# Kernel optimization log

Measured on AMD Instinct MI355X. Metric: run time of the kernel, lower is better.

The kernel has to match this reference:

```python
import jax, jax.numpy as jnp
import numpy as np
import math

N, V, NH = 4096, 256, 64  # samples, variables (channels), hidden units


def _permutation_skeleton(v):
    # perm[c] is a (V, V-1) selection matrix keeping all variables j != c,
    # columns ordered by j (faithful to CustomizedRelaModule.permutation_matrix
    # with skeleton = 1 - I, so max_dim = V - 1 and no zero-padding remains).
    perm = np.zeros((v, v, v - 1), dtype=np.float32)
    for c in range(v):
        idx = np.delete(np.arange(v), c)
        perm[c, idx, np.arange(v - 1)] = 1.0
    return jnp.asarray(perm)


def setup_inputs() -> dict:
    key = jax.random.key(0)
    k = jax.random.split(key, 7)
    data = jax.random.normal(k[0], (N, V), dtype=jnp.float32)
    adj = jax.random.normal(k[1], (V, V), dtype=jnp.float32)        # self.adj_matrix ~ N(0,1)
    neurons = jax.random.normal(k[2], (NH, V), dtype=jnp.float32)   # self.neurons ~ N(0,1)
    s1 = 1.0 / math.sqrt(V - 1)  # input_layer: uniform(-1/sqrt(in), 1/sqrt(in)), in = max_dim = V-1
    w_in = jax.random.uniform(k[3], (V, V - 1, NH), minval=-s1, maxval=s1, dtype=jnp.float32)
    b_in = jax.random.uniform(k[4], (V, NH), minval=-s1, maxval=s1, dtype=jnp.float32)
    s2 = 1.0 / math.sqrt(NH)
    w_out = jax.random.uniform(k[5], (V, NH, 1), minval=-s2, maxval=s2, dtype=jnp.float32)
    b_out = jax.random.uniform(k[6], (V, 1), minval=-s2, maxval=s2, dtype=jnp.float32)
    perm = _permutation_skeleton(V)
    return {"data": data, "adj": adj, "neurons": neurons,
            "w_in": w_in, "b_in": b_in, "w_out": w_out, "b_out": b_out,
            "perm": perm}


def reference(data, adj, neurons, w_in, b_in, w_out, b_out, perm):
    # categorical_matrix is identity, so the adjacency passed is adj itself.
    # Linear3D input layer with adj + permutation:
    #   masked[n, c, k] = sum_j data[n, j] * adj[j, c] * perm[c, j, k]
    # i.e. per channel c, gather adj-weighted inputs for all j != c.
    masked = jnp.einsum('nj,jc,cjk->nck', data, adj, perm)  # (N, V, V-1)
    # per-channel linear + tanh
    h = jnp.tanh(jnp.einsum('nck,ckh->nch', masked, w_in) + b_in[None])  # (N, V, NH)
    # output Linear3D with adj_matrix = neurons (NH, V): elementwise gate then per-channel linear
    gated = h * neurons.T[None]  # (N, V, NH)
    out = jnp.einsum('nch,cho->nco', gated, w_out) + b_out[None]  # (N, V, 1)
    return (adj, out[..., 0])
```

## Files before the change

kernel.cpp:

```cpp
#include <hip/hip_runtime.h>
#include <hip/hip_bf16.h>

#define NS   4096
#define NV   256
#define NHID 64
#define K2F  2.8853900817779268f

typedef short s8v __attribute__((ext_vector_type(8)));
typedef float f4v __attribute__((ext_vector_type(4)));

typedef __attribute__((address_space(1))) const unsigned int GU;
typedef __attribute__((address_space(3))) unsigned int LU;

__device__ __forceinline__ void gload16(const void* gp, void* lp) {
    __builtin_amdgcn_global_load_lds((GU*)gp, (LU*)lp, 16, 0, 0);
}

__device__ __forceinline__ unsigned short f2bf(float x) {
    __hip_bfloat16 h = __float2bfloat16(x);
    return *reinterpret_cast<unsigned short*>(&h);
}

__global__ __launch_bounds__(256) void k_prep_w2t(const float* __restrict__ adj,
                                                  const float* __restrict__ w_in,
                                                  unsigned short* __restrict__ W2t) {
    __shared__ float t[64][65];
    int c  = blockIdx.x >> 2;
    int k0 = (blockIdx.x & 3) * 64;
    int tid = threadIdx.x;
#pragma unroll
    for (int i = 0; i < 16; ++i) {
        int lin = i * 256 + tid;
        int kr = lin >> 6, h = lin & 63;
        int k = k0 + kr;
        float v = 0.0f;
        if (k != c) {
            int m = k - (k > c ? 1 : 0);
            v = adj[k * NV + c] * w_in[((size_t)c * 255 + m) * 64 + h];
        }
        t[kr][h] = v;
    }
    __syncthreads();
#pragma unroll
    for (int i = 0; i < 16; ++i) {
        int lin = i * 256 + tid;
        int h = lin >> 6, kr = lin & 63;
        W2t[((size_t)(c * 64 + h)) * NV + k0 + kr] = f2bf(t[kr][h]);
    }
}

__global__ __launch_bounds__(256) void k_prep_small(
        const float* __restrict__ data, unsigned short* __restrict__ dataB,
        const float* __restrict__ adj,  float* __restrict__ out0,
        const float* __restrict__ neurons, const float* __restrict__ w_out,
        const float* __restrict__ b_out, float* __restrict__ g2, float* __restrict__ BO,
        const float* __restrict__ b_in, float* __restrict__ bi2)
{
    const int b = blockIdx.x, tid = threadIdx.x;
    if (b < 1024) {
        int i = b * 256 + tid;
        float4 v = reinterpret_cast<const float4*>(data)[i];
        ushort4 o = make_ushort4(f2bf(v.x), f2bf(v.y), f2bf(v.z), f2bf(v.w));
        reinterpret_cast<ushort4*>(dataB)[i] = o;
    } else if (b < 1088) {
        int i = (b - 1024) * 256 + tid;
        reinterpret_cast<float4*>(out0)[i] = reinterpret_cast<const float4*>(adj)[i];
    } else if (b < 1152) {
        int j = (b - 1088) * 256 + tid;
        int c = j >> 6, h = j & 63;
        float gv = neurons[h * NV + c] * w_out[j];
        g2[j] = 2.0f * gv;
        float s = gv;
        s += __shfl_xor(s, 1);  s += __shfl_xor(s, 2);  s += __shfl_xor(s, 4);
        s += __shfl_xor(s, 8);  s += __shfl_xor(s, 16); s += __shfl_xor(s, 32);
        if ((tid & 63) == 0) BO[c] = b_out[c] + s;
    } else {
        int i = (b - 1152) * 256 + tid;
        float4 v = reinterpret_cast<const float4*>(b_in)[i];
        v.x *= K2F; v.y *= K2F; v.z *= K2F; v.w *= K2F;
        reinterpret_cast<float4*>(bi2)[i] = v;
    }
}

__global__ __launch_bounds__(256, 3) void k_gemm_fused(
        const unsigned short* __restrict__ dataB,
        const unsigned short* __restrict__ W2t,
        const float* __restrict__ g2,
        const float* __restrict__ bi2,
        const float* __restrict__ BO,
        float* __restrict__ out1)
{
    __shared__ __align__(16) char lds[32768];
    const int tid  = threadIdx.x;
    const int w    = tid >> 6;
    const int lane = tid & 63;
    const int lq   = lane >> 4, lr = lane & 15;
    const int wr   = w >> 1, wc = w & 1;

    const int orig = (int)blockIdx.x;
    const int swz  = (orig & 7) * 512 + (orig >> 3);
    const int bm0  = (swz & 31) << 7;
    const int bn0  = (swz >> 5) << 7;

    f4v acc[4][4];
#pragma unroll
    for (int mi = 0; mi < 4; ++mi)
#pragma unroll
        for (int ni = 0; ni < 4; ++ni)
            acc[mi][ni] = (f4v){0.f, 0.f, 0.f, 0.f};

    unsigned int offA[4], offB[4], ldso[4];
#pragma unroll
    for (int t = 0; t < 4; ++t) {
        int o = w * 4096 + t * 1024 + lane * 16;
        int row = o >> 7;
        int inner = (o & 127) ^ ((row & 7) << 4);
        ldso[t] = (unsigned)(w * 4096 + t * 1024);
        offA[t] = (unsigned)(bm0 + row) * 512u + (unsigned)inner;
        offB[t] = (unsigned)(bn0 + row) * 512u + (unsigned)inner;
    }

    const char* dA = (const char*)dataB;
    const char* dB = (const char*)W2t;

    for (int kt = 0; kt < 4; ++kt) {
#pragma unroll
        for (int t = 0; t < 4; ++t)
            gload16(dA + (size_t)offA[t] + kt * 128, lds + ldso[t]);
#pragma unroll
        for (int t = 0; t < 4; ++t)
            gload16(dB + (size_t)offB[t] + kt * 128, lds + 16384 + ldso[t]);
        __syncthreads();

#pragma unroll
        for (int kk = 0; kk < 2; ++kk) {
            s8v afr[4], bfr[4];
#pragma unroll
            for (int mi = 0; mi < 4; ++mi) {
                int ml = wr * 64 + mi * 16 + lr;
                int inner = (kk * 64 + (lq << 4)) ^ ((ml & 7) << 4);
                afr[mi] = *reinterpret_cast<const s8v*>(lds + ml * 128 + inner);
            }
#pragma unroll
            for (int ni = 0; ni < 4; ++ni) {
                int nl = wc * 64 + ni * 16 + lr;
                int inner = (kk * 64 + (lq << 4)) ^ ((nl & 7) << 4);
                bfr[ni] = *reinterpret_cast<const s8v*>(lds + 16384 + nl * 128 + inner);
            }
            __builtin_amdgcn_s_setprio(1);
#pragma unroll
            for (int mi = 0; mi < 4; ++mi)
#pragma unroll
                for (int ni = 0; ni < 4; ++ni)
                    acc[mi][ni] = __builtin_amdgcn_mfma_f32_16x16x32_bf16(
                        bfr[ni], afr[mi], acc[mi][ni], 0, 0, 0);
            __builtin_amdgcn_s_setprio(0);
        }
        __syncthreads();
    }

    const int cidx = (bn0 >> 6) + wc;
    float4 g2v[4], bi2v[4];
#pragma unroll
    for (int ni = 0; ni < 4; ++ni) {
        int base = cidx * 64 + ni * 16 + lq * 4;
        g2v[ni]  = *(const float4*)&g2 [base];
        bi2v[ni] = *(const float4*)&bi2[base];
    }
    const float BOv = BO[cidx];

    float s0, s1, s2, s3;
#define EPI_TERM(T, GC, BC, RR)                                                \
    { float mm = __builtin_fmaf(acc[mi][ni][RR], K2F, (BC));                   \
      float e  = __builtin_amdgcn_exp2f(mm);                                   \
      (T) = __builtin_fmaf((GC), __builtin_amdgcn_rcpf(e + 1.0f), (T)); }
#define EPI_MI(T)                                                              \
    { float t = 0.f;                                                           \
      _Pragma("unroll")                                                        \
      for (int ni = 0; ni < 4; ++ni) {                                         \
          EPI_TERM(t, g2v[ni].x, bi2v[ni].x, 0);                               \
          EPI_TERM(t, g2v[ni].y, bi2v[ni].y, 1);                               \
          EPI_TERM(t, g2v[ni].z, bi2v[ni].z, 2);                               \
          EPI_TERM(t, g2v[ni].w, bi2v[ni].w, 3);                               \
      }                                                                        \
      t += __shfl_xor(t, 16);                                                  \
      t += __shfl_xor(t, 32);                                                  \
      (T) = t; }
    { const int mi = 0; EPI_MI(s0); }
    { const int mi = 1; EPI_MI(s1); }
    { const int mi = 2; EPI_MI(s2); }
    { const int mi = 3; EPI_MI(s3); }
#undef EPI_MI
#undef EPI_TERM
    float v = lane < 16 ? s0 : (lane < 32 ? s1 : (lane < 48 ? s2 : s3));
    out1[(unsigned)(bm0 + wr * 64 + lane) * NV + cidx] = BOv - v;
}

extern "C" void kernel_launch(void* const* d_in, const int* in_sizes, int n_in,
                              void* d_out, int out_size, void* d_ws, size_t ws_size,
                              hipStream_t stream) {
    const float* data    = (const float*)d_in[0];
    const float* adj     = (const float*)d_in[1];
    const float* neurons = (const float*)d_in[2];
    const float* w_in    = (const float*)d_in[3];
    const float* b_in    = (const float*)d_in[4];
    const float* w_out   = (const float*)d_in[5];
    const float* b_out   = (const float*)d_in[6];

    float* out0 = (float*)d_out;
    float* out1 = out0 + NV * NV;

    unsigned short* dataB = (unsigned short*)d_ws;
    unsigned short* W2t   = (unsigned short*)((char*)d_ws + 2097152);
    float*          g2    = (float*)((char*)d_ws + 10485760);
    float*          bi2   = (float*)((char*)d_ws + 10551296);
    float*          BO    = (float*)((char*)d_ws + 10616832);

    hipLaunchKernelGGL(k_prep_w2t,   dim3(1024), dim3(256), 0, stream, adj, w_in, W2t);
    hipLaunchKernelGGL(k_prep_small, dim3(1168), dim3(256), 0, stream,
                       data, dataB, adj, out0, neurons, w_out, b_out, g2, BO, b_in, bi2);
    hipLaunchKernelGGL(k_gemm_fused, dim3(4096), dim3(256), 0, stream,
                       dataB, W2t, g2, bi2, BO, out1);
}
```

Before: 62.33 us.

## Merge prep kernels and triple-buffer GEMM K-loop with async LDS loads

The two preprocessing kernels are merged into one launch, dropping a kernel boundary. The GEMM main loop moves from 4 single-buffered K-steps of 64 elements with two syncthreads each to 8 K-steps of 32 elements in a 3-stage LDS ring. Prefetch runs two stages ahead, using vmcnt waits and a single barrier per step. This overlaps global-to-LDS loads with MFMA work, but raises LDS per block to 48KB, which may lower occupancy, and it removes the XOR swizzle, so LDS bank conflicts may appear.

```diff
diff --git a/kernel.cpp b/kernel.cpp
--- a/kernel.cpp
+++ b/kernel.cpp
@@ -21,42 +21,42 @@
     return *reinterpret_cast<unsigned short*>(&h);
 }
 
-__global__ __launch_bounds__(256) void k_prep_w2t(const float* __restrict__ adj,
-                                                  const float* __restrict__ w_in,
-                                                  unsigned short* __restrict__ W2t) {
-    __shared__ float t[64][65];
-    int c  = blockIdx.x >> 2;
-    int k0 = (blockIdx.x & 3) * 64;
-    int tid = threadIdx.x;
-#pragma unroll
-    for (int i = 0; i < 16; ++i) {
-        int lin = i * 256 + tid;
-        int kr = lin >> 6, h = lin & 63;
-        int k = k0 + kr;
-        float v = 0.0f;
-        if (k != c) {
-            int m = k - (k > c ? 1 : 0);
-            v = adj[k * NV + c] * w_in[((size_t)c * 255 + m) * 64 + h];
-        }
-        t[kr][h] = v;
-    }
-    __syncthreads();
-#pragma unroll
-    for (int i = 0; i < 16; ++i) {
-        int lin = i * 256 + tid;
-        int h = lin >> 6, kr = lin & 63;
-        W2t[((size_t)(c * 64 + h)) * NV + k0 + kr] = f2bf(t[kr][h]);
-    }
-}
-
-__global__ __launch_bounds__(256) void k_prep_small(
+__global__ __launch_bounds__(256) void k_prep_all(
+        const float* __restrict__ adj, const float* __restrict__ w_in,
+        unsigned short* __restrict__ W2t,
         const float* __restrict__ data, unsigned short* __restrict__ dataB,
-        const float* __restrict__ adj,  float* __restrict__ out0,
+        float* __restrict__ out0,
         const float* __restrict__ neurons, const float* __restrict__ w_out,
         const float* __restrict__ b_out, float* __restrict__ g2, float* __restrict__ BO,
         const float* __restrict__ b_in, float* __restrict__ bi2)
 {
-    const int b = blockIdx.x, tid = threadIdx.x;
+    __shared__ float t[64][65];
+    const int blk = blockIdx.x, tid = threadIdx.x;
+    if (blk < 1024) {
+        int c  = blk >> 2;
+        int k0 = (blk & 3) * 64;
+#pragma unroll
+        for (int i = 0; i < 16; ++i) {
+            int lin = i * 256 + tid;
+            int kr = lin >> 6, h = lin & 63;
+            int k = k0 + kr;
+            float v = 0.0f;
+            if (k != c) {
+                int m = k - (k > c ? 1 : 0);
+                v = adj[k * NV + c] * w_in[((size_t)c * 255 + m) * 64 + h];
+            }
+            t[kr][h] = v;
+        }
+        __syncthreads();
+#pragma unroll
+        for (int i = 0; i < 16; ++i) {
+            int lin = i * 256 + tid;
+            int h = lin >> 6, kr = lin & 63;
+            W2t[((size_t)(c * 64 + h)) * NV + k0 + kr] = f2bf(t[kr][h]);
+        }
+        return;
+    }
+    const int b = blk - 1024;
     if (b < 1024) {
         int i = b * 256 + tid;
         float4 v = reinterpret_cast<const float4*>(data)[i];
@@ -90,7 +90,7 @@
         const float* __restrict__ BO,
         float* __restrict__ out1)
 {
-    __shared__ __align__(16) char lds[32768];
+    __shared__ __align__(16) char lds[49152];
     const int tid  = threadIdx.x;
     const int w    = tid >> 6;
     const int lane = tid & 63;
@@ -109,55 +109,56 @@
         for (int ni = 0; ni < 4; ++ni)
             acc[mi][ni] = (f4v){0.f, 0.f, 0.f, 0.f};
 
-    unsigned int offA[4], offB[4], ldso[4];
-#pragma unroll
-    for (int t = 0; t < 4; ++t) {
-        int o = w * 4096 + t * 1024 + lane * 16;
-        int row = o >> 7;
-        int inner = (o & 127) ^ ((row & 7) << 4);
-        ldso[t] = (unsigned)(w * 4096 + t * 1024);
-        offA[t] = (unsigned)(bm0 + row) * 512u + (unsigned)inner;
-        offB[t] = (unsigned)(bn0 + row) * 512u + (unsigned)inner;
-    }
-
     const char* dA = (const char*)dataB;
     const char* dB = (const char*)W2t;
-
-    for (int kt = 0; kt < 4; ++kt) {
-#pragma unroll
-        for (int t = 0; t < 4; ++t)
-            gload16(dA + (size_t)offA[t] + kt * 128, lds + ldso[t]);
-#pragma unroll
-        for (int t = 0; t < 4; ++t)
-            gload16(dB + (size_t)offB[t] + kt * 128, lds + 16384 + ldso[t]);
-        __syncthreads();
-
-#pragma unroll
-        for (int kk = 0; kk < 2; ++kk) {
-            s8v afr[4], bfr[4];
-#pragma unroll
-            for (int mi = 0; mi < 4; ++mi) {
-                int ml = wr * 64 + mi * 16 + lr;
-                int inner = (kk * 64 + (lq << 4)) ^ ((ml & 7) << 4);
-                afr[mi] = *reinterpret_cast<const s8v*>(lds + ml * 128 + inner);
-            }
-#pragma unroll
-            for (int ni = 0; ni < 4; ++ni) {
-                int nl = wc * 64 + ni * 16 + lr;
-                int inner = (kk * 64 + (lq << 4)) ^ ((nl & 7) << 4);
-                bfr[ni] = *reinterpret_cast<const s8v*>(lds + 16384 + nl * 128 + inner);
-            }
-            __builtin_amdgcn_s_setprio(1);
-#pragma unroll
-            for (int mi = 0; mi < 4; ++mi)
-#pragma unroll
-                for (int ni = 0; ni < 4; ++ni)
-                    acc[mi][ni] = __builtin_amdgcn_mfma_f32_16x16x32_bf16(
-                        bfr[ni], afr[mi], acc[mi][ni], 0, 0, 0);
-            __builtin_amdgcn_s_setprio(0);
-        }
-        __syncthreads();
-    }
+    const int rowt = tid >> 2;
+    const int colb = (tid & 3) * 16;
+    const char* srcA = dA + (size_t)(bm0 + rowt) * 512 + colb;
+    const char* srcB = dB + (size_t)(bn0 + rowt) * 512 + colb;
+    const unsigned ldst = (unsigned)(rowt * 64 + colb);
+
+#define STAGE(KT, BUFO)                                                        \
+    do {                                                                       \
+        gload16(srcA + (KT) * 64,         lds + (BUFO) + ldst);                \
+        gload16(srcA + 32768 + (KT) * 64, lds + (BUFO) + 4096 + ldst);         \
+        gload16(srcB + (KT) * 64,         lds + (BUFO) + 8192 + ldst);         \
+        gload16(srcB + 32768 + (KT) * 64, lds + (BUFO) + 12288 + ldst);        \
+    } while (0)
+
+    STAGE(0, 0);
+    STAGE(1, 16384);
+
+#pragma unroll
+    for (int kt = 0; kt < 8; ++kt) {
+        const int bufo = (kt % 3) * 16384;
+        if (kt < 7) { asm volatile("s_waitcnt vmcnt(4)" ::: "memory"); }
+        else        { asm volatile("s_waitcnt vmcnt(0)" ::: "memory"); }
+        __builtin_amdgcn_sched_barrier(0);
+        __builtin_amdgcn_s_barrier();
+        __builtin_amdgcn_sched_barrier(0);
+        if (kt < 6) STAGE(kt + 2, ((kt + 2) % 3) * 16384);
+
+        s8v afr[4], bfr[4];
+#pragma unroll
+        for (int mi = 0; mi < 4; ++mi) {
+            int ml = wr * 64 + mi * 16 + lr;
+            afr[mi] = *reinterpret_cast<const s8v*>(lds + bufo + ml * 64 + lq * 16);
+        }
+#pragma unroll
+        for (int ni = 0; ni < 4; ++ni) {
+            int nl = wc * 64 + ni * 16 + lr;
+            bfr[ni] = *reinterpret_cast<const s8v*>(lds + bufo + 8192 + nl * 64 + lq * 16);
+        }
+        __builtin_amdgcn_s_setprio(1);
+#pragma unroll
+        for (int mi = 0; mi < 4; ++mi)
+#pragma unroll
+            for (int ni = 0; ni < 4; ++ni)
+                acc[mi][ni] = __builtin_amdgcn_mfma_f32_16x16x32_bf16(
+                    bfr[ni], afr[mi], acc[mi][ni], 0, 0, 0);
+        __builtin_amdgcn_s_setprio(0);
+    }
+#undef STAGE
 
     const int cidx = (bn0 >> 6) + wc;
     float4 g2v[4], bi2v[4];
@@ -216,9 +217,9 @@
     float*          bi2   = (float*)((char*)d_ws + 10551296);
     float*          BO    = (float*)((char*)d_ws + 10616832);
 
-    hipLaunchKernelGGL(k_prep_w2t,   dim3(1024), dim3(256), 0, stream, adj, w_in, W2t);
-    hipLaunchKernelGGL(k_prep_small, dim3(1168), dim3(256), 0, stream,
-                       data, dataB, adj, out0, neurons, w_out, b_out, g2, BO, b_in, bi2);
+    hipLaunchKernelGGL(k_prep_all, dim3(2192), dim3(256), 0, stream,
+                       adj, w_in, W2t, data, dataB, out0,
+                       neurons, w_out, b_out, g2, BO, b_in, bi2);
     hipLaunchKernelGGL(k_gemm_fused, dim3(4096), dim3(256), 0, stream,
                        dataB, W2t, g2, bi2, BO, out1);
 }
```

Result: faster. 60.02 us (-3.7%).

## Merge prep kernels and widen GEMM tile to 128x256 with 8x4 per-wave accumulators

Applied to the files above, without the earlier changes.

The two preprocessing kernels become one launch that dispatches on block index, removing one kernel launch and its gap. The fused GEMM tile grows from 128x128 to 128x256. Each wave now covers all 128 rows and 64 columns (one channel), which halves the grid and cuts reloads of the A operand. The cost is more registers for 32 accumulators, occupancy bound lowered from 3 to 2, and larger LDS use at 48KB.

```diff
diff --git a/kernel.cpp b/kernel.cpp
--- a/kernel.cpp
+++ b/kernel.cpp
@@ -21,42 +21,42 @@
     return *reinterpret_cast<unsigned short*>(&h);
 }
 
-__global__ __launch_bounds__(256) void k_prep_w2t(const float* __restrict__ adj,
-                                                  const float* __restrict__ w_in,
-                                                  unsigned short* __restrict__ W2t) {
-    __shared__ float t[64][65];
-    int c  = blockIdx.x >> 2;
-    int k0 = (blockIdx.x & 3) * 64;
-    int tid = threadIdx.x;
-#pragma unroll
-    for (int i = 0; i < 16; ++i) {
-        int lin = i * 256 + tid;
-        int kr = lin >> 6, h = lin & 63;
-        int k = k0 + kr;
-        float v = 0.0f;
-        if (k != c) {
-            int m = k - (k > c ? 1 : 0);
-            v = adj[k * NV + c] * w_in[((size_t)c * 255 + m) * 64 + h];
-        }
-        t[kr][h] = v;
-    }
-    __syncthreads();
-#pragma unroll
-    for (int i = 0; i < 16; ++i) {
-        int lin = i * 256 + tid;
-        int h = lin >> 6, kr = lin & 63;
-        W2t[((size_t)(c * 64 + h)) * NV + k0 + kr] = f2bf(t[kr][h]);
-    }
-}
-
-__global__ __launch_bounds__(256) void k_prep_small(
+__global__ __launch_bounds__(256) void k_prep_all(
+        const float* __restrict__ adj, const float* __restrict__ w_in,
+        unsigned short* __restrict__ W2t,
         const float* __restrict__ data, unsigned short* __restrict__ dataB,
-        const float* __restrict__ adj,  float* __restrict__ out0,
+        float* __restrict__ out0,
         const float* __restrict__ neurons, const float* __restrict__ w_out,
         const float* __restrict__ b_out, float* __restrict__ g2, float* __restrict__ BO,
         const float* __restrict__ b_in, float* __restrict__ bi2)
 {
-    const int b = blockIdx.x, tid = threadIdx.x;
+    __shared__ float t[64][65];
+    const int blk = blockIdx.x, tid = threadIdx.x;
+    if (blk < 1024) {
+        int c  = blk >> 2;
+        int k0 = (blk & 3) * 64;
+#pragma unroll
+        for (int i = 0; i < 16; ++i) {
+            int lin = i * 256 + tid;
+            int kr = lin >> 6, h = lin & 63;
+            int k = k0 + kr;
+            float v = 0.0f;
+            if (k != c) {
+                int m = k - (k > c ? 1 : 0);
+                v = adj[k * NV + c] * w_in[((size_t)c * 255 + m) * 64 + h];
+            }
+            t[kr][h] = v;
+        }
+        __syncthreads();
+#pragma unroll
+        for (int i = 0; i < 16; ++i) {
+            int lin = i * 256 + tid;
+            int h = lin >> 6, kr = lin & 63;
+            W2t[((size_t)(c * 64 + h)) * NV + k0 + kr] = f2bf(t[kr][h]);
+        }
+        return;
+    }
+    const int b = blk - 1024;
     if (b < 1024) {
         int i = b * 256 + tid;
         float4 v = reinterpret_cast<const float4*>(data)[i];
@@ -82,7 +82,7 @@
     }
 }
 
-__global__ __launch_bounds__(256, 3) void k_gemm_fused(
+__global__ __launch_bounds__(256, 2) void k_gemm_fused(
         const unsigned short* __restrict__ dataB,
         const unsigned short* __restrict__ W2t,
         const float* __restrict__ g2,
@@ -90,34 +90,40 @@
         const float* __restrict__ BO,
         float* __restrict__ out1)
 {
-    __shared__ __align__(16) char lds[32768];
+    __shared__ __align__(16) char lds[49152];
     const int tid  = threadIdx.x;
     const int w    = tid >> 6;
     const int lane = tid & 63;
     const int lq   = lane >> 4, lr = lane & 15;
-    const int wr   = w >> 1, wc = w & 1;
 
     const int orig = (int)blockIdx.x;
-    const int swz  = (orig & 7) * 512 + (orig >> 3);
+    const int swz  = (orig & 7) * 256 + (orig >> 3);
     const int bm0  = (swz & 31) << 7;
-    const int bn0  = (swz >> 5) << 7;
-
-    f4v acc[4][4];
-#pragma unroll
-    for (int mi = 0; mi < 4; ++mi)
+    const int bn0  = (swz >> 5) << 8;
+
+    f4v acc[8][4];
+#pragma unroll
+    for (int mi = 0; mi < 8; ++mi)
 #pragma unroll
         for (int ni = 0; ni < 4; ++ni)
             acc[mi][ni] = (f4v){0.f, 0.f, 0.f, 0.f};
 
-    unsigned int offA[4], offB[4], ldso[4];
+    unsigned int offA[4], ldsoA[4], offB[8], ldsoB[8];
 #pragma unroll
     for (int t = 0; t < 4; ++t) {
         int o = w * 4096 + t * 1024 + lane * 16;
         int row = o >> 7;
         int inner = (o & 127) ^ ((row & 7) << 4);
-        ldso[t] = (unsigned)(w * 4096 + t * 1024);
-        offA[t] = (unsigned)(bm0 + row) * 512u + (unsigned)inner;
-        offB[t] = (unsigned)(bn0 + row) * 512u + (unsigned)inner;
+        ldsoA[t] = (unsigned)(w * 4096 + t * 1024);
+        offA[t]  = (unsigned)(bm0 + row) * 512u + (unsigned)inner;
+    }
+#pragma unroll
+    for (int t = 0; t < 8; ++t) {
+        int o = w * 8192 + t * 1024 + lane * 16;
+        int row = o >> 7;
+        int inner = (o & 127) ^ ((row & 7) << 4);
+        ldsoB[t] = (unsigned)(16384 + w * 8192 + t * 1024);
+        offB[t]  = (unsigned)(bn0 + row) * 512u + (unsigned)inner;
     }
 
     const char* dA = (const char*)dataB;
@@ -126,30 +132,30 @@
     for (int kt = 0; kt < 4; ++kt) {
 #pragma unroll
         for (int t = 0; t < 4; ++t)
-            gload16(dA + (size_t)offA[t] + kt * 128, lds + ldso[t]);
-#pragma unroll
-        for (int t = 0; t < 4; ++t)
-            gload16(dB + (size_t)offB[t] + kt * 128, lds + 16384 + ldso[t]);
+            gload16(dA + (size_t)offA[t] + kt * 128, lds + ldsoA[t]);
+#pragma unroll
+        for (int t = 0; t < 8; ++t)
+            gload16(dB + (size_t)offB[t] + kt * 128, lds + ldsoB[t]);
         __syncthreads();
 
 #pragma unroll
         for (int kk = 0; kk < 2; ++kk) {
-            s8v afr[4], bfr[4];
-#pragma unroll
-            for (int mi = 0; mi < 4; ++mi) {
-                int ml = wr * 64 + mi * 16 + lr;
+            s8v afr[8], bfr[4];
+#pragma unroll
+            for (int mi = 0; mi < 8; ++mi) {
+                int ml = mi * 16 + lr;
                 int inner = (kk * 64 + (lq << 4)) ^ ((ml & 7) << 4);
                 afr[mi] = *reinterpret_cast<const s8v*>(lds + ml * 128 + inner);
             }
 #pragma unroll
             for (int ni = 0; ni < 4; ++ni) {
-                int nl = wc * 64 + ni * 16 + lr;
+                int nl = w * 64 + ni * 16 + lr;
                 int inner = (kk * 64 + (lq << 4)) ^ ((nl & 7) << 4);
                 bfr[ni] = *reinterpret_cast<const s8v*>(lds + 16384 + nl * 128 + inner);
             }
             __builtin_amdgcn_s_setprio(1);
 #pragma unroll
-            for (int mi = 0; mi < 4; ++mi)
+            for (int mi = 0; mi < 8; ++mi)
 #pragma unroll
                 for (int ni = 0; ni < 4; ++ni)
                     acc[mi][ni] = __builtin_amdgcn_mfma_f32_16x16x32_bf16(
@@ -159,7 +165,7 @@
         __syncthreads();
     }
 
-    const int cidx = (bn0 >> 6) + wc;
+    const int cidx = (bn0 >> 6) + w;
     float4 g2v[4], bi2v[4];
 #pragma unroll
     for (int ni = 0; ni < 4; ++ni) {
@@ -169,13 +175,13 @@
     }
     const float BOv = BO[cidx];
 
-    float s0, s1, s2, s3;
+    float s0, s1, s2, s3, s4, s5, s6, s7;
 #define EPI_TERM(T, GC, BC, RR)                                                \
     { float mm = __builtin_fmaf(acc[mi][ni][RR], K2F, (BC));                   \
       float e  = __builtin_amdgcn_exp2f(mm);                                   \
       (T) = __builtin_fmaf((GC), __builtin_amdgcn_rcpf(e + 1.0f), (T)); }
-#define EPI_MI(T)                                                              \
-    { float t = 0.f;                                                           \
+#define EPI_MI(T, MI)                                                          \
+    { const int mi = (MI); float t = 0.f;                                      \
       _Pragma("unroll")                                                        \
       for (int ni = 0; ni < 4; ++ni) {                                         \
           EPI_TERM(t, g2v[ni].x, bi2v[ni].x, 0);                               \
@@ -186,14 +192,14 @@
       t += __shfl_xor(t, 16);                                                  \
       t += __shfl_xor(t, 32);                                                  \
       (T) = t; }
-    { const int mi = 0; EPI_MI(s0); }
-    { const int mi = 1; EPI_MI(s1); }
-    { const int mi = 2; EPI_MI(s2); }
-    { const int mi = 3; EPI_MI(s3); }
+    EPI_MI(s0, 0); EPI_MI(s1, 1); EPI_MI(s2, 2); EPI_MI(s3, 3);
+    EPI_MI(s4, 4); EPI_MI(s5, 5); EPI_MI(s6, 6); EPI_MI(s7, 7);
 #undef EPI_MI
 #undef EPI_TERM
-    float v = lane < 16 ? s0 : (lane < 32 ? s1 : (lane < 48 ? s2 : s3));
-    out1[(unsigned)(bm0 + wr * 64 + lane) * NV + cidx] = BOv - v;
+    float vlo = lane < 16 ? s0 : (lane < 32 ? s1 : (lane < 48 ? s2 : s3));
+    float vhi = lane < 16 ? s4 : (lane < 32 ? s5 : (lane < 48 ? s6 : s7));
+    out1[(unsigned)(bm0 + lane) * NV + cidx]      = BOv - vlo;
+    out1[(unsigned)(bm0 + 64 + lane) * NV + cidx] = BOv - vhi;
 }
 
 extern "C" void kernel_launch(void* const* d_in, const int* in_sizes, int n_in,
@@ -216,9 +222,9 @@
     float*          bi2   = (float*)((char*)d_ws + 10551296);
     float*          BO    = (float*)((char*)d_ws + 10616832);
 
-    hipLaunchKernelGGL(k_prep_w2t,   dim3(1024), dim3(256), 0, stream, adj, w_in, W2t);
-    hipLaunchKernelGGL(k_prep_small, dim3(1168), dim3(256), 0, stream,
-                       data, dataB, adj, out0, neurons, w_out, b_out, g2, BO, b_in, bi2);
-    hipLaunchKernelGGL(k_gemm_fused, dim3(4096), dim3(256), 0, stream,
+    hipLaunchKernelGGL(k_prep_all, dim3(2192), dim3(256), 0, stream,
+                       adj, w_in, W2t, data, dataB, out0,
+                       neurons, w_out, b_out, g2, BO, b_in, bi2);
+    hipLaunchKernelGGL(k_gemm_fused, dim3(2048), dim3(256), 0, stream,
                        dataB, W2t, g2, bi2, BO, out1);
 }
```

After: 55.87 us, median of 2. -10.4%, faster.
